# Kernel tuning notes

Hardware: AMD Instinct MI355X
Metric: run time of the kernel (lower is better)

## Reference

```python
import jax, jax.numpy as jnp
import numpy as np

N = 100000
E = 1600000
F_IN, HID, N_CLS = 128, 16, 32


def setup_inputs() -> dict:
    key = jax.random.key(0)
    ks = jax.random.split(key, 10)
    x = jax.random.normal(ks[0], (N, F_IN), dtype=jnp.float32)
    edge_index = jax.random.randint(ks[1], (2, E), 0, N, dtype=jnp.int64)
    edge_weight = jax.random.uniform(ks[2], (E,), dtype=jnp.float32)
    def glorot(k, shape):
        lim = np.sqrt(6.0 / (shape[0] + shape[1])).astype(np.float32)
        return jax.random.uniform(k, shape, dtype=jnp.float32, minval=-lim, maxval=lim)
    return {
        'x': x, 'edge_index': edge_index, 'edge_weight': edge_weight,
        'W1_0': glorot(ks[3], (F_IN, HID)), 'W1_1': glorot(ks[4], (F_IN, HID)),
        'b1': jnp.zeros((HID,), jnp.float32),
        'W2_0': glorot(ks[5], (HID, N_CLS)), 'W2_1': glorot(ks[6], (HID, N_CLS)),
        'b2': jnp.zeros((N_CLS,), jnp.float32),
    }


def _cheb_conv_k2(x, row, col, edge_weight, W0, W1, b):
    # PyG ChebConv, K=2, lambda_max=2.0:
    #   T0 = x; T1 = L_hat x = D^{-1/2} A D^{-1/2} x - x
    n = x.shape[0]
    deg = jax.ops.segment_sum(edge_weight, row, num_segments=n)  # [N]
    dinv = jnp.where(deg > 0, jax.lax.rsqrt(deg), 0.0)
    norm = dinv[row] * edge_weight * dinv[col]                   # [E]
    agg = jax.ops.segment_sum(norm[:, None] * x[col], row, num_segments=n)  # [N,F]
    tx1 = agg - x
    return x @ W0 + tx1 @ W1 + b


def reference(x, edge_index, edge_weight, W1_0, W1_1, b1, W2_0, W2_1, b2):
    row, col = edge_index[0], edge_index[1]
    h = jax.nn.relu(_cheb_conv_k2(x, row, col, edge_weight, W1_0, W1_1, b1))
    # dropout(p=0) and DFA layers are identity in forward
    out = _cheb_conv_k2(h, row, col, edge_weight, W2_0, W2_1, b2)
    return jax.nn.log_softmax(out, axis=1)
```

## Files before the change

### kernel.cpp

```cpp
#include <hip/hip_runtime.h>
#include <hip/hip_bf16.h>


#include <hip/hip_fp16.h>

constexpr int NN   = 100000;
constexpr int NE   = 1600000;
constexpr int FIN  = 128;
constexpr int HID  = 16;
constexpr int NCLS = 32;

constexpr int RB    = 256;
constexpr int NBKT  = (NN + RB - 1) / RB;
constexpr int EPB   = 4096;
constexpr int EPT   = EPB / 256;
constexpr int GP    = (NE + EPB - 1) / EPB;
constexpr int CAP   = 8192;

typedef float f32x2 __attribute__((ext_vector_type(2)));

#if defined(__has_builtin)
#if __has_builtin(__builtin_amdgcn_cvt_pk_f32_fp8)
#define HAVE_CVT_FP8 1
#endif
#endif

static __device__ __forceinline__ unsigned int f2e4m3(float f) {
    union { float f; unsigned int u; } v; v.f = f;
    unsigned int s = (v.u >> 24) & 0x80u;
    unsigned int au = v.u & 0x7fffffffu;
    if (au > 0x43E00000u) au = 0x43E00000u;
    au += 0x7ffffu + ((au >> 20) & 1u);
    int e4 = (int)(au >> 23) - 120;
    unsigned int m = (au >> 20) & 7u;
    unsigned int byte = (e4 <= 0) ? 0u : (((unsigned int)e4 << 3) | m);
    return s | byte;
}
static __device__ __forceinline__ void fp8x4_fma(unsigned int v, float w, float* acc) {
#ifdef HAVE_CVT_FP8
    f32x2 lo = __builtin_amdgcn_cvt_pk_f32_fp8((int)v, false);
    f32x2 hi = __builtin_amdgcn_cvt_pk_f32_fp8((int)v, true);
    acc[0] += w * lo.x; acc[1] += w * lo.y;
    acc[2] += w * hi.x; acc[3] += w * hi.y;
#else
#pragma unroll
    for (int i = 0; i < 4; i++) {
        unsigned int b = (v >> (8 * i)) & 0xffu;
        float f = __int_as_float((int)(((b & 0x80u) << 24) | ((b & 0x7fu) << 20))) * 0x1p120f;
        acc[i] += w * f;
    }
#endif
}
static __device__ __forceinline__ unsigned int wpack(float wf) {
    unsigned int b = __float_as_uint(wf) + 0x8000u;
    return (b >> 16) & 0x7fffu;
}
static __device__ __forceinline__ float wdec(unsigned int u) {
    return __uint_as_float((u >> 17) << 16);
}

__global__ void k_zero_cur(int* __restrict__ bucketCursor) {
    int i = blockIdx.x * blockDim.x + threadIdx.x;
    if (i < NBKT) bucketCursor[i] = 0;
}

__global__ __launch_bounds__(256) void k_partition(
    const int* __restrict__ row, const int* __restrict__ col,
    const float* __restrict__ w, int* __restrict__ bucketCursor,
    int2* __restrict__ partS) {
    __shared__ int2 stage[EPB];
    __shared__ unsigned short sbkt[EPB];
    __shared__ int cnt[NBKT];
    __shared__ int lofs[NBKT];
    __shared__ int cursor[NBKT];
    __shared__ int gbase[NBKT];
    __shared__ int sa[512], sb[512];
    int tid = threadIdx.x;
    long ebase = (long)blockIdx.x * EPB;
    int rr[EPT]; int cc[EPT]; float wv[EPT];
#pragma unroll
    for (int i = 0; i < EPT; i++) {
        long e = ebase + i * 256 + tid;
        if (e < NE) { rr[i] = row[e]; cc[i] = col[e]; wv[i] = w[e]; }
        else rr[i] = -1;
    }
    for (int i = tid; i < NBKT; i += 256) cnt[i] = 0;
    __syncthreads();
#pragma unroll
    for (int i = 0; i < EPT; i++)
        if (rr[i] >= 0) atomicAdd(&cnt[rr[i] >> 8], 1);
    __syncthreads();
    for (int i = tid; i < 512; i += 256) sa[i] = (i < NBKT) ? cnt[i] : 0;
    __syncthreads();
    int* src = sa; int* dst = sb;
    for (int off = 1; off < 512; off <<= 1) {
        for (int i = tid; i < 512; i += 256)
            dst[i] = src[i] + ((i >= off) ? src[i - off] : 0);
        __syncthreads();
        int* t = src; src = dst; dst = t;
    }
    for (int i = tid; i < NBKT; i += 256) {
        int ex = src[i] - cnt[i];
        lofs[i] = ex;
        cursor[i] = ex;
        int go = (cnt[i] > 0) ? atomicAdd(&bucketCursor[i], cnt[i]) : 0;
        gbase[i] = i * CAP + go;
    }
    __syncthreads();
#pragma unroll
    for (int i = 0; i < EPT; i++) {
        if (rr[i] >= 0) {
            int b = rr[i] >> 8;
            int p = atomicAdd(&cursor[b], 1);
            int2 v;
            v.x = cc[i] | ((rr[i] & 255) << 17);
            v.y = __float_as_int(wv[i]);
            stage[p] = v;
            sbkt[p] = (unsigned short)b;
        }
    }
    __syncthreads();
    int total = (int)min((long)EPB, NE - ebase);
    for (int i = tid; i < total; i += 256) {
        int b = sbkt[i];
        partS[gbase[b] + (i - lofs[b])] = stage[i];
    }
}

__global__ void k_scan_buckets(const int* __restrict__ bucketCursor,
                               int* __restrict__ bucketStart) {
    int lane = threadIdx.x;
    int v[8], e[8];
    int s = 0;
#pragma unroll
    for (int t = 0; t < 8; t++) {
        int idx = lane * 8 + t;
        v[t] = (idx < NBKT) ? bucketCursor[idx] : 0;
        e[t] = s;
        s += v[t];
    }
    int sc = s;
    for (int off = 1; off < 64; off <<= 1) {
        int up = __shfl_up(sc, off, 64);
        if (lane >= off) sc += up;
    }
    int excl = sc - s;
#pragma unroll
    for (int t = 0; t < 8; t++) {
        int idx = lane * 8 + t;
        if (idx < NBKT) bucketStart[idx] = excl + e[t];
    }
}

__global__ __launch_bounds__(256) void k_bucket_sort(
    const int2* __restrict__ partS, const int* __restrict__ bucketCursor,
    const int* __restrict__ bucketStart,
    unsigned int* __restrict__ partC, int* __restrict__ rowptr,
    float* __restrict__ dinv) {
    __shared__ int2 stage[CAP];
    __shared__ int hist[RB];
    __shared__ int cursor[RB];
    __shared__ int wtot[4];
    int b = blockIdx.x;
    int tid = threadIdx.x;
    int start = bucketStart[b];
    int count = bucketCursor[b];
    const int2* src = partS + (long)b * CAP;
    hist[tid] = 0;
    __syncthreads();
    for (int i = tid; i < count; i += 256)
        atomicAdd(&hist[(src[i].x >> 17) & 255], 1);
    __syncthreads();
    int lane = tid & 63, wv = tid >> 6;
    int v = hist[tid];
    int sc = v;
#pragma unroll
    for (int off = 1; off < 64; off <<= 1) {
        int up = __shfl_up(sc, off, 64);
        if (lane >= off) sc += up;
    }
    if (lane == 63) wtot[wv] = sc;
    __syncthreads();
    int add = 0;
    for (int w2 = 0; w2 < wv; w2++) add += wtot[w2];
    int ex = sc + add - v;
    int node = b * RB + tid;
    if (node <= NN) rowptr[node] = start + ex;
    cursor[tid] = ex;
    __syncthreads();
    for (int i = tid; i < count; i += 256) {
        int2 p = src[i];
        int rl = (p.x >> 17) & 255;
        int pos = atomicAdd(&cursor[rl], 1);
        int2 c; c.x = p.x & 0x1FFFF; c.y = p.y;
        if (pos < CAP) stage[pos] = c;
    }
    __syncthreads();
    {
        int rend = cursor[tid];
        float d = 0.f;
        for (int i = ex; i < rend; i++) d += __int_as_float(stage[i].y);
        if (node < NN) dinv[node] = d > 0.f ? rsqrtf(d) : 0.f;
    }
    for (int i = tid; i < count; i += 256)
        if (i < CAP) {
            int2 p = stage[i];
            partC[start + i] = (unsigned int)p.x | (wpack(__int_as_float(p.y)) << 17);
        }
}

__global__ __launch_bounds__(128) void k_proj1(
    const float* __restrict__ x, const float* __restrict__ W0,
    const float* __restrict__ W1, const float* __restrict__ b1,
    const float* __restrict__ dinv,
    float* __restrict__ xa, unsigned char* __restrict__ xb8) {
    long t = (long)blockIdx.x * 128 + threadIdx.x;
    bool valid = t < NN;
    long n = valid ? t : 0;
    const float4* xg = (const float4*)x + n * 32;
    float accA[HID], accB[HID];
#pragma unroll
    for (int o = 0; o < HID; o++) { accA[o] = 0.f; accB[o] = 0.f; }
    float4 bufA[8], bufB[8];
#pragma unroll
    for (int m = 0; m < 8; m++) bufA[m] = xg[m];
#pragma unroll
    for (int m = 0; m < 8; m++) bufB[m] = xg[8 + m];

#define PROJ1_CHUNK(BUF, C)                                            \
    {                                                                   \
        const float* W0p = W0 + (C) * 32 * HID;                         \
        const float* W1p = W1 + (C) * 32 * HID;                         \
        _Pragma("unroll")                                               \
        for (int m = 0; m < 8; m++) {                                   \
            float xv[4] = {BUF[m].x, BUF[m].y, BUF[m].z, BUF[m].w};     \
            _Pragma("unroll")                                           \
            for (int q = 0; q < 4; q++) {                               \
                int k = m * 4 + q;                                      \
                _Pragma("unroll")                                       \
                for (int o = 0; o < HID; o++) accA[o] += xv[q] * W0p[k * HID + o]; \
                _Pragma("unroll")                                       \
                for (int o = 0; o < HID; o++) accB[o] += xv[q] * W1p[k * HID + o]; \
            }                                                           \
        }                                                               \
    }

    PROJ1_CHUNK(bufA, 0)
#pragma unroll
    for (int m = 0; m < 8; m++) bufA[m] = xg[16 + m];
    PROJ1_CHUNK(bufB, 1)
#pragma unroll
    for (int m = 0; m < 8; m++) bufB[m] = xg[24 + m];
    PROJ1_CHUNK(bufA, 2)
    PROJ1_CHUNK(bufB, 3)
#undef PROJ1_CHUNK

    if (!valid) return;
    float4* xap = (float4*)(xa + n * HID);
#pragma unroll
    for (int q = 0; q < 4; q++) {
        float4 va;
        va.x = accA[4*q+0] - accB[4*q+0] + b1[4*q+0];
        va.y = accA[4*q+1] - accB[4*q+1] + b1[4*q+1];
        va.z = accA[4*q+2] - accB[4*q+2] + b1[4*q+2];
        va.w = accA[4*q+3] - accB[4*q+3] + b1[4*q+3];
        xap[q] = va;
    }
    float dn = dinv[n];
    unsigned int pk[4];
#pragma unroll
    for (int q = 0; q < 4; q++)
        pk[q] = f2e4m3(dn * accB[4*q+0]) | (f2e4m3(dn * accB[4*q+1]) << 8)
              | (f2e4m3(dn * accB[4*q+2]) << 16) | (f2e4m3(dn * accB[4*q+3]) << 24);
    *(uint4*)(xb8 + n * HID) = make_uint4(pk[0], pk[1], pk[2], pk[3]);
}

__global__ __launch_bounds__(256) void k_gather1(
    const int* __restrict__ rowptr, const unsigned int* __restrict__ partC,
    const float* __restrict__ dinv, const unsigned char* __restrict__ xb8,
    float* __restrict__ agg1) {
    long t = (long)blockIdx.x * 256 + threadIdx.x;
    int n = (int)(t >> 6);
    if (n >= NN) return;
    int lane = threadIdx.x & 63;
    int d = lane & 3, p = lane >> 2;
    int s = rowptr[n], e = rowptr[n + 1];
    float acc[4] = {0.f, 0.f, 0.f, 0.f};
    for (int j = s + p; j < e; j += 16) {
        unsigned int u = partC[j];
        unsigned int v = *(const unsigned int*)(xb8 + (u & 0x1FFFF) * HID + d * 4);
        fp8x4_fma(v, wdec(u), acc);
    }
#pragma unroll
    for (int i = 0; i < 4; i++) {
        acc[i] += __shfl_xor(acc[i], 4);
        acc[i] += __shfl_xor(acc[i], 8);
        acc[i] += __shfl_xor(acc[i], 16);
        acc[i] += __shfl_xor(acc[i], 32);
    }
    if (p == 0) {
        float dn = dinv[n];
        float4 o; o.x = dn * acc[0]; o.y = dn * acc[1];
        o.z = dn * acc[2]; o.w = dn * acc[3];
        *(float4*)(agg1 + (long)n * HID + d * 4) = o;
    }
}

__global__ __launch_bounds__(256) void k_proj2(
    const float* __restrict__ xa, const float* __restrict__ agg1,
    const float* __restrict__ W0, const float* __restrict__ W1,
    const float* __restrict__ b2, const float* __restrict__ dinv,
    float* __restrict__ ha, unsigned char* __restrict__ hb8) {
    long n = (long)blockIdx.x * 256 + threadIdx.x;
    if (n >= NN) return;
    float h[HID];
    const float4* xap = (const float4*)(xa + n * HID);
    const float4* agp = (const float4*)(agg1 + n * HID);
#pragma unroll
    for (int q = 0; q < 4; q++) {
        float4 a = xap[q], g = agp[q];
        h[4*q+0] = fmaxf(a.x + g.x, 0.f);
        h[4*q+1] = fmaxf(a.y + g.y, 0.f);
        h[4*q+2] = fmaxf(a.z + g.z, 0.f);
        h[4*q+3] = fmaxf(a.w + g.w, 0.f);
    }
    float accA[NCLS], accB[NCLS];
#pragma unroll
    for (int o = 0; o < NCLS; o++) { accA[o] = 0.f; accB[o] = 0.f; }
#pragma unroll 2
    for (int k = 0; k < HID; k++) {
        float hk = h[k];
#pragma unroll
        for (int o = 0; o < NCLS; o++) accA[o] += hk * W0[k * NCLS + o];
#pragma unroll
        for (int o = 0; o < NCLS; o++) accB[o] += hk * W1[k * NCLS + o];
    }
    float4* hap = (float4*)(ha + n * NCLS);
#pragma unroll
    for (int q = 0; q < 8; q++) {
        float4 va;
        va.x = accA[4*q+0] - accB[4*q+0] + b2[4*q+0];
        va.y = accA[4*q+1] - accB[4*q+1] + b2[4*q+1];
        va.z = accA[4*q+2] - accB[4*q+2] + b2[4*q+2];
        va.w = accA[4*q+3] - accB[4*q+3] + b2[4*q+3];
        hap[q] = va;
    }
    float dn = dinv[n];
    unsigned int pk[8];
#pragma unroll
    for (int q = 0; q < 8; q++)
        pk[q] = f2e4m3(dn * accB[4*q+0]) | (f2e4m3(dn * accB[4*q+1]) << 8)
              | (f2e4m3(dn * accB[4*q+2]) << 16) | (f2e4m3(dn * accB[4*q+3]) << 24);
    uint4* hbp = (uint4*)(hb8 + n * NCLS);
    hbp[0] = make_uint4(pk[0], pk[1], pk[2], pk[3]);
    hbp[1] = make_uint4(pk[4], pk[5], pk[6], pk[7]);
}

__global__ __launch_bounds__(256) void k_gather2_lsm(
    const int* __restrict__ rowptr, const unsigned int* __restrict__ partC,
    const float* __restrict__ dinv, const float* __restrict__ ha,
    const unsigned char* __restrict__ hb8, float* __restrict__ out) {
    long t = (long)blockIdx.x * 256 + threadIdx.x;
    int n = (int)(t >> 6);
    if (n >= NN) return;
    int lane = threadIdx.x & 63;
    int d = lane & 7, p = lane >> 3;
    int s = rowptr[n], e = rowptr[n + 1];
    float acc[4] = {0.f, 0.f, 0.f, 0.f};
    int j = s + p;
    for (; j + 8 < e; j += 16) {
        unsigned int u0 = partC[j], u1 = partC[j + 8];
        unsigned int v0 = *(const unsigned int*)(hb8 + (u0 & 0x1FFFF) * NCLS + d * 4);
        unsigned int v1 = *(const unsigned int*)(hb8 + (u1 & 0x1FFFF) * NCLS + d * 4);
        fp8x4_fma(v0, wdec(u0), acc);
        fp8x4_fma(v1, wdec(u1), acc);
    }
    if (j < e) {
        unsigned int u0 = partC[j];
        unsigned int v0 = *(const unsigned int*)(hb8 + (u0 & 0x1FFFF) * NCLS + d * 4);
        fp8x4_fma(v0, wdec(u0), acc);
    }
#pragma unroll
    for (int i = 0; i < 4; i++) {
        acc[i] += __shfl_xor(acc[i], 8);
        acc[i] += __shfl_xor(acc[i], 16);
        acc[i] += __shfl_xor(acc[i], 32);
    }
    float dn = dinv[n];
    float4 hv = *(const float4*)(ha + (long)n * NCLS + d * 4);
    float v0 = dn * acc[0] + hv.x;
    float v1 = dn * acc[1] + hv.y;
    float v2 = dn * acc[2] + hv.z;
    float v3 = dn * acc[3] + hv.w;
    float m = fmaxf(fmaxf(v0, v1), fmaxf(v2, v3));
    m = fmaxf(m, __shfl_xor(m, 1));
    m = fmaxf(m, __shfl_xor(m, 2));
    m = fmaxf(m, __shfl_xor(m, 4));
    float sum = __expf(v0 - m) + __expf(v1 - m) + __expf(v2 - m) + __expf(v3 - m);
    sum += __shfl_xor(sum, 1);
    sum += __shfl_xor(sum, 2);
    sum += __shfl_xor(sum, 4);
    float ls = logf(sum);
    if (p == 0) {
        float4 o; o.x = v0 - m - ls; o.y = v1 - m - ls;
        o.z = v2 - m - ls; o.w = v3 - m - ls;
        *(float4*)(out + (long)n * NCLS + d * 4) = o;
    }
}

extern "C" void kernel_launch(void* const* d_in, const int* in_sizes, int n_in,
                              void* d_out, int out_size, void* d_ws, size_t ws_size,
                              hipStream_t stream) {
    const float* x    = (const float*)d_in[0];
    const int*   ei   = (const int*)d_in[1];
    const float* ew   = (const float*)d_in[2];
    const float* W1_0 = (const float*)d_in[3];
    const float* W1_1 = (const float*)d_in[4];
    const float* b1   = (const float*)d_in[5];
    const float* W2_0 = (const float*)d_in[6];
    const float* W2_1 = (const float*)d_in[7];
    const float* b2   = (const float*)d_in[8];
    float* out = (float*)d_out;

    const int* row = ei;
    const int* col = ei + NE;

    char* ws = (char*)d_ws;
    int2*  partS     = (int2*)ws;                 ws += sizeof(int2) * (long)NBKT * CAP;
    unsigned int* partC = (unsigned int*)ws;      ws += sizeof(int) * NE;
    int*   bucketCursor = (int*)ws;               ws += sizeof(int) * NBKT;
    int*   bucketStart  = (int*)ws;               ws += sizeof(int) * NBKT;
    int*   rowptr    = (int*)ws;                  ws += sizeof(int) * (NN + 4);
    float* dinv      = (float*)ws;                ws += sizeof(float) * NN;
    float* xa        = (float*)ws;                ws += sizeof(float) * NN * HID;
    float* agg1      = (float*)ws;                ws += sizeof(float) * NN * HID;
    float* ha        = (float*)ws;                ws += sizeof(float) * NN * NCLS;
    unsigned char* xb8 = (unsigned char*)ws;      ws += sizeof(char) * NN * HID;
    unsigned char* hb8 = (unsigned char*)ws;      ws += sizeof(char) * NN * NCLS;

    k_zero_cur<<<(NBKT + 255) / 256, 256, 0, stream>>>(bucketCursor);
    k_partition<<<GP, 256, 0, stream>>>(row, col, ew, bucketCursor, partS);
    k_scan_buckets<<<1, 64, 0, stream>>>(bucketCursor, bucketStart);
    k_bucket_sort<<<NBKT, 256, 0, stream>>>(partS, bucketCursor, bucketStart,
                                            partC, rowptr, dinv);
    k_proj1<<<(NN + 127) / 128, 128, 0, stream>>>(x, W1_0, W1_1, b1, dinv, xa, xb8);
    {
        long th = (long)NN * 64;
        k_gather1<<<(int)((th + 255) / 256), 256, 0, stream>>>(rowptr, partC, dinv, xb8, agg1);
    }
    k_proj2<<<(NN + 255) / 256, 256, 0, stream>>>(xa, agg1, W2_0, W2_1, b2, dinv, ha, hb8);
    {
        long th = (long)NN * 64;
        k_gather2_lsm<<<(int)((th + 255) / 256), 256, 0, stream>>>(rowptr, partC, dinv, ha, hb8, out);
    }
}
```

Baseline: 249.1 us.

## Compute first-layer projection with bf16 MFMA tiles instead of scalar FMAs

Rewrites the x@W projection kernel so each wavefront handles a 16-node tile and uses 16x16x32 bf16 MFMA instructions against both weight matrices. Inputs and weights are rounded to bf16 in registers, which replaces a long chain of per-thread scalar FMAs over 128x32 weights. This lowers precision from fp32 to bf16 products and stores outputs as scattered per-element writes instead of vector stores. The kernel reads 51 MB of x, so it is probably bandwidth-bound and the compute saving may matter less than the load pattern.

```diff
diff --git a/kernel.cpp b/kernel.cpp
--- a/kernel.cpp
+++ b/kernel.cpp
@@ -16,8 +16,11 @@
 constexpr int EPT   = EPB / 256;
 constexpr int GP    = (NE + EPB - 1) / EPB;
 constexpr int CAP   = 8192;
+constexpr int NTILE = NN / 16;
 
 typedef float f32x2 __attribute__((ext_vector_type(2)));
+typedef float f32x4 __attribute__((ext_vector_type(4)));
+typedef short bf16x8 __attribute__((ext_vector_type(8)));
 
 #if defined(__has_builtin)
 #if __has_builtin(__builtin_amdgcn_cvt_pk_f32_fp8)
@@ -50,6 +53,11 @@
         acc[i] += w * f;
     }
 #endif
+}
+static __device__ __forceinline__ unsigned short f2bf(float f) {
+    union { float f; unsigned int u; } v; v.f = f;
+    unsigned int r = v.u + 0x7fffu + ((v.u >> 16) & 1u);
+    return (unsigned short)(r >> 16);
 }
 static __device__ __forceinline__ unsigned int wpack(float wf) {
     unsigned int b = __float_as_uint(wf) + 0x8000u;
@@ -209,70 +217,59 @@
         }
 }
 
-__global__ __launch_bounds__(128) void k_proj1(
+__global__ __launch_bounds__(256) void k_proj1(
     const float* __restrict__ x, const float* __restrict__ W0,
     const float* __restrict__ W1, const float* __restrict__ b1,
     const float* __restrict__ dinv,
     float* __restrict__ xa, unsigned char* __restrict__ xb8) {
-    long t = (long)blockIdx.x * 128 + threadIdx.x;
-    bool valid = t < NN;
-    long n = valid ? t : 0;
-    const float4* xg = (const float4*)x + n * 32;
-    float accA[HID], accB[HID];
-#pragma unroll
-    for (int o = 0; o < HID; o++) { accA[o] = 0.f; accB[o] = 0.f; }
-    float4 bufA[8], bufB[8];
-#pragma unroll
-    for (int m = 0; m < 8; m++) bufA[m] = xg[m];
-#pragma unroll
-    for (int m = 0; m < 8; m++) bufB[m] = xg[8 + m];
-
-#define PROJ1_CHUNK(BUF, C)                                            \
-    {                                                                   \
-        const float* W0p = W0 + (C) * 32 * HID;                         \
-        const float* W1p = W1 + (C) * 32 * HID;                         \
-        _Pragma("unroll")                                               \
-        for (int m = 0; m < 8; m++) {                                   \
-            float xv[4] = {BUF[m].x, BUF[m].y, BUF[m].z, BUF[m].w};     \
-            _Pragma("unroll")                                           \
-            for (int q = 0; q < 4; q++) {                               \
-                int k = m * 4 + q;                                      \
-                _Pragma("unroll")                                       \
-                for (int o = 0; o < HID; o++) accA[o] += xv[q] * W0p[k * HID + o]; \
-                _Pragma("unroll")                                       \
-                for (int o = 0; o < HID; o++) accB[o] += xv[q] * W1p[k * HID + o]; \
-            }                                                           \
-        }                                                               \
-    }
-
-    PROJ1_CHUNK(bufA, 0)
-#pragma unroll
-    for (int m = 0; m < 8; m++) bufA[m] = xg[16 + m];
-    PROJ1_CHUNK(bufB, 1)
-#pragma unroll
-    for (int m = 0; m < 8; m++) bufB[m] = xg[24 + m];
-    PROJ1_CHUNK(bufA, 2)
-    PROJ1_CHUNK(bufB, 3)
-#undef PROJ1_CHUNK
-
-    if (!valid) return;
-    float4* xap = (float4*)(xa + n * HID);
-#pragma unroll
-    for (int q = 0; q < 4; q++) {
-        float4 va;
-        va.x = accA[4*q+0] - accB[4*q+0] + b1[4*q+0];
-        va.y = accA[4*q+1] - accB[4*q+1] + b1[4*q+1];
-        va.z = accA[4*q+2] - accB[4*q+2] + b1[4*q+2];
-        va.w = accA[4*q+3] - accB[4*q+3] + b1[4*q+3];
-        xap[q] = va;
-    }
-    float dn = dinv[n];
-    unsigned int pk[4];
-#pragma unroll
-    for (int q = 0; q < 4; q++)
-        pk[q] = f2e4m3(dn * accB[4*q+0]) | (f2e4m3(dn * accB[4*q+1]) << 8)
-              | (f2e4m3(dn * accB[4*q+2]) << 16) | (f2e4m3(dn * accB[4*q+3]) << 24);
-    *(uint4*)(xb8 + n * HID) = make_uint4(pk[0], pk[1], pk[2], pk[3]);
+    int wid = (int)(((long)blockIdx.x * 256 + threadIdx.x) >> 6);
+    if (wid >= NTILE) return;
+    int lane = threadIdx.x & 63;
+    int col = lane & 15, quad = lane >> 4;
+
+    bf16x8 bfrag[2][4];
+#pragma unroll
+    for (int mat = 0; mat < 2; mat++) {
+        const float* W = mat ? W1 : W0;
+#pragma unroll
+        for (int kb = 0; kb < 4; kb++) {
+            bf16x8 f;
+#pragma unroll
+            for (int j = 0; j < 8; j++)
+                f[j] = (short)f2bf(W[(kb * 32 + quad * 8 + j) * HID + col]);
+            bfrag[mat][kb] = f;
+        }
+    }
+
+    const float* xrow = x + ((long)wid * 16 + col) * FIN + quad * 8;
+    float4 xb[8];
+#pragma unroll
+    for (int kb = 0; kb < 4; kb++) {
+        xb[2 * kb]     = *(const float4*)(xrow + kb * 32);
+        xb[2 * kb + 1] = *(const float4*)(xrow + kb * 32 + 4);
+    }
+    f32x4 acc0 = {0.f, 0.f, 0.f, 0.f}, acc1 = {0.f, 0.f, 0.f, 0.f};
+#pragma unroll
+    for (int kb = 0; kb < 4; kb++) {
+        float4 a0 = xb[2 * kb], a1 = xb[2 * kb + 1];
+        bf16x8 af;
+        af[0] = (short)f2bf(a0.x); af[1] = (short)f2bf(a0.y);
+        af[2] = (short)f2bf(a0.z); af[3] = (short)f2bf(a0.w);
+        af[4] = (short)f2bf(a1.x); af[5] = (short)f2bf(a1.y);
+        af[6] = (short)f2bf(a1.z); af[7] = (short)f2bf(a1.w);
+        acc0 = __builtin_amdgcn_mfma_f32_16x16x32_bf16(af, bfrag[0][kb], acc0, 0, 0, 0);
+        acc1 = __builtin_amdgcn_mfma_f32_16x16x32_bf16(af, bfrag[1][kb], acc1, 0, 0, 0);
+    }
+
+    float b1v = b1[col];
+#pragma unroll
+    for (int r = 0; r < 4; r++) {
+        long node = (long)wid * 16 + quad * 4 + r;
+        float a0 = acc0[r], a1 = acc1[r];
+        xa[node * HID + col] = a0 - a1 + b1v;
+        float dn = dinv[node];
+        xb8[node * HID + col] = (unsigned char)f2e4m3(dn * a1);
+    }
 }
 
 __global__ __launch_bounds__(256) void k_gather1(
@@ -443,7 +440,7 @@
     k_scan_buckets<<<1, 64, 0, stream>>>(bucketCursor, bucketStart);
     k_bucket_sort<<<NBKT, 256, 0, stream>>>(partS, bucketCursor, bucketStart,
                                             partC, rowptr, dinv);
-    k_proj1<<<(NN + 127) / 128, 128, 0, stream>>>(x, W1_0, W1_1, b1, dinv, xa, xb8);
+    k_proj1<<<(NTILE * 64 + 255) / 256, 256, 0, stream>>>(x, W1_0, W1_1, b1, dinv, xa, xb8);
     {
         long th = (long)NN * 64;
         k_gather1<<<(int)((th + 255) / 256), 256, 0, stream>>>(rowptr, partC, dinv, xb8, agg1);
```

Measured after the change: 232.5 us. 6.7% less time.
